# Optimization experiments

Hardware: AMD Instinct MI355X
Metric: run time of the kernel (lower is better)

## Reference

```python
import jax, jax.numpy as jnp
import numpy as np

N_NODES = 50000
N_EDGES = 400000
D = 64        # hidden_features
H_NE = 16     # hidden_ne_features
L = 4         # num_layers
EPS = 1e-5


def _ln(z, g, b):
    # layer norm over feature dim
    mu = jnp.mean(z, axis=-1, keepdims=True)
    var = jnp.var(z, axis=-1, keepdims=True)
    return (z - mu) * jax.lax.rsqrt(var + EPS) * g + b


def setup_inputs() -> dict:
    key = jax.random.key(0)
    ks = iter(jax.random.split(key, 64))
    def rn(shape, s=0.05):
        return jax.random.normal(next(ks), shape, dtype=jnp.float32) * s
    inp = {
        "x": rn((N_NODES, 2), 1.0),
        "e": rn((N_EDGES, 2), 1.0),
        "src": jax.random.randint(next(ks), (N_EDGES,), 0, N_NODES, dtype=jnp.int32),
        "dst": jax.random.randint(next(ks), (N_EDGES,), 0, N_NODES, dtype=jnp.int32),
        # node / edge encoders (2-layer MLPs)
        "ne_W1": rn((2, H_NE)), "ne_b1": jnp.zeros((H_NE,), jnp.float32),
        "ne_W2": rn((H_NE, D)), "ne_b2": jnp.zeros((D,), jnp.float32),
        "ee_W1": rn((2, H_NE)), "ee_b1": jnp.zeros((H_NE,), jnp.float32),
        "ee_W2": rn((H_NE, D)), "ee_b2": jnp.zeros((D,), jnp.float32),
        # stacked per-layer GatedGCN weights
        "A1": rn((L, D, D)), "bA1": jnp.zeros((L, D), jnp.float32),
        "A2": rn((L, D, D)), "bA2": jnp.zeros((L, D), jnp.float32),
        "A3": rn((L, D, D)), "bA3": jnp.zeros((L, D), jnp.float32),
        "B1": rn((L, D, D)), "bB1": jnp.zeros((L, D), jnp.float32),
        "B2": rn((L, D, D)), "bB2": jnp.zeros((L, D), jnp.float32),
        "B3": rn((L, D, D)), "bB3": jnp.zeros((L, D), jnp.float32),
        "ge": jnp.ones((L, D), jnp.float32), "be": jnp.zeros((L, D), jnp.float32),
        "gh": jnp.ones((L, D), jnp.float32), "bh": jnp.zeros((L, D), jnp.float32),
        # score predictor
        "pW1": rn((3 * D, D)), "pb1": jnp.zeros((D,), jnp.float32),
        "pW2": rn((D, 1)), "pb2": jnp.zeros((1,), jnp.float32),
    }
    return inp


def _forward(x, e, src, dst,
             ne_W1, ne_b1, ne_W2, ne_b2,
             ee_W1, ee_b1, ee_W2, ee_b2,
             A1, bA1, A2, bA2, A3, bA3,
             B1, bB1, B2, bB2, B3, bB3,
             ge, be, gh, bh,
             pW1, pb1, pW2, pb2):
    # encoders
    x = jax.nn.relu(x @ ne_W1 + ne_b1) @ ne_W2 + ne_b2      # [N, D]
    e = jax.nn.relu(e @ ee_W1 + ee_b1) @ ee_W2 + ee_b2      # [E, D]

    params = {"A1": A1, "bA1": bA1, "A2": A2, "bA2": bA2,
              "A3": A3, "bA3": bA3, "B1": B1, "bB1": bB1,
              "B2": B2, "bB2": bB2, "B3": B3, "bB3": bB3,
              "ge": ge, "be": be, "gh": gh, "bh": bh}

    def layer(carry, p):
        x, e = carry
        # edge update: e_ij += ReLU(LN(B1 h_i + B2 h_j + B3 e_ij))
        e_hat = (x[src] @ p["B1"] + p["bB1"]
                 + x[dst] @ p["B2"] + p["bB2"]
                 + e @ p["B3"] + p["bB3"])                  # [E, D]
        e = e + jax.nn.relu(_ln(e_hat, p["ge"], p["be"]))
        sigma = jax.nn.sigmoid(e)                             # gates [E, D]
        # directed aggregation: forward (src->dst) and backward (dst->src)
        a2 = x @ p["A2"] + p["bA2"]
        a3 = x @ p["A3"] + p["bA3"]
        m_f = jax.ops.segment_sum(sigma * a2[src], dst, num_segments=N_NODES)
        d_f = jax.ops.segment_sum(sigma, dst, num_segments=N_NODES)
        m_b = jax.ops.segment_sum(sigma * a3[dst], src, num_segments=N_NODES)
        d_b = jax.ops.segment_sum(sigma, src, num_segments=N_NODES)
        h = (x @ p["A1"] + p["bA1"]
             + m_f / (d_f + EPS) + m_b / (d_b + EPS))        # [N, D]
        x = x + jax.nn.relu(_ln(h, p["gh"], p["bh"]))
        return (x, e), None

    (x, e), _ = jax.lax.scan(layer, (x, e), params)

    # score predictor: MLP over cat(x_src, x_dst, e)
    z = jnp.concatenate([x[src], x[dst], e], axis=-1)        # [E, 3D]
    return jax.nn.relu(z @ pW1 + pb1) @ pW2 + pb2            # [E, 1]


def reference(x, e, src, dst,
              ne_W1, ne_b1, ne_W2, ne_b2,
              ee_W1, ee_b1, ee_W2, ee_b2,
              A1, bA1, A2, bA2, A3, bA3,
              B1, bB1, B2, bB2, B3, bB3,
              ge, be, gh, bh,
              pW1, pb1, pW2, pb2):
    return _forward(x, e, src, dst,
                    ne_W1, ne_b1, ne_W2, ne_b2,
                    ee_W1, ee_b1, ee_W2, ee_b2,
                    A1, bA1, A2, bA2, A3, bA3,
                    B1, bB1, B2, bB2, B3, bB3,
                    ge, be, gh, bh,
                    pW1, pb1, pW2, pb2)
```

## Files before the change

kernel.cpp:

```cpp
#include <hip/hip_runtime.h>

#define N_NODES 50000
#define N_EDGES 400000
#define EPSV 1e-5f
#define SCAN_BLK 49
#define SCAN_PAD (49 * 1024)

__global__ __launch_bounds__(256) void encode_kernel(
    const float* __restrict__ in2, const float* __restrict__ W1,
    const float* __restrict__ b1, const float* __restrict__ W2,
    const float* __restrict__ b2, float* __restrict__ out, int nrows)
{
  int t = blockIdx.x * 256 + threadIdx.x;
  int row = t >> 4;
  int d0 = t & 15;
  if (row >= nrows) return;
  float x0 = in2[row * 2 + 0], x1 = in2[row * 2 + 1];
  float h[16];
#pragma unroll
  for (int j = 0; j < 16; ++j)
    h[j] = fmaxf(fmaf(x0, W1[j], fmaf(x1, W1[16 + j], b1[j])), 0.f);
#pragma unroll
  for (int q = 0; q < 4; ++q) {
    int d = d0 + q * 16;
    float a = b2[d];
#pragma unroll
    for (int j = 0; j < 16; ++j) a = fmaf(h[j], W2[j * 64 + d], a);
    out[(size_t)row * 64 + d] = a;
  }
}

__global__ __launch_bounds__(256) void encode_perm_kernel(
    const float* __restrict__ in2, const float* __restrict__ W1,
    const float* __restrict__ b1, const float* __restrict__ W2,
    const float* __restrict__ b2, const int2* __restrict__ csr_f,
    float* __restrict__ out)
{
  int t = blockIdx.x * 256 + threadIdx.x;
  int row = t >> 4;
  int d0 = t & 15;
  if (row >= N_EDGES) return;
  int orig = csr_f[row].x;
  float x0 = in2[orig * 2 + 0], x1 = in2[orig * 2 + 1];
  float h[16];
#pragma unroll
  for (int j = 0; j < 16; ++j)
    h[j] = fmaxf(fmaf(x0, W1[j], fmaf(x1, W1[16 + j], b1[j])), 0.f);
#pragma unroll
  for (int q = 0; q < 4; ++q) {
    int d = d0 + q * 16;
    float a = b2[d];
#pragma unroll
    for (int j = 0; j < 16; ++j) a = fmaf(h[j], W2[j * 64 + d], a);
    out[(size_t)row * 64 + d] = a;
  }
}

__global__ __launch_bounds__(256) void hist_kernel(
    const int* __restrict__ src, const int* __restrict__ dst,
    int* __restrict__ cnt_f, int* __restrict__ cnt_b)
{
  int t = blockIdx.x * 256 + threadIdx.x;
  if (t >= N_EDGES) return;
  atomicAdd(&cnt_f[dst[t]], 1);
  atomicAdd(&cnt_b[src[t]], 1);
}

__global__ __launch_bounds__(1024) void scanA_kernel(
    const int* __restrict__ cnt_f, const int* __restrict__ cnt_b,
    int* __restrict__ part, int* __restrict__ bsum)
{
  int dir = blockIdx.x / SCAN_BLK;
  int blk = blockIdx.x % SCAN_BLK;
  const int* cnt = dir ? cnt_b : cnt_f;
  int t = threadIdx.x;
  int idx = blk * 1024 + t;
  int v = (idx < N_NODES) ? cnt[idx] : 0;
  __shared__ int sh[1024];
  sh[t] = v;
  __syncthreads();
  for (int o = 1; o < 1024; o <<= 1) {
    int u = (t >= o) ? sh[t - o] : 0;
    __syncthreads();
    sh[t] += u;
    __syncthreads();
  }
  part[dir * SCAN_PAD + idx] = sh[t] - v;
  if (t == 1023) bsum[dir * SCAN_BLK + blk] = sh[1023];
}

__global__ __launch_bounds__(64) void scanB_kernel(
    int* __restrict__ bsum, int* __restrict__ off_f, int* __restrict__ off_b)
{
  int t = threadIdx.x;
  if (t < 2) {
    int* b = bsum + t * SCAN_BLK;
    int run = 0;
    for (int i = 0; i < SCAN_BLK; ++i) {
      int v = b[i];
      b[i] = run;
      run += v;
    }
    if (t == 0) off_f[N_NODES] = run;
    else off_b[N_NODES] = run;
  }
}

__global__ __launch_bounds__(1024) void scanC_kernel(
    const int* __restrict__ part, const int* __restrict__ bsum,
    int* __restrict__ off_f, int* __restrict__ off_b,
    int* __restrict__ cur_f, int* __restrict__ cur_b)
{
  int dir = blockIdx.x / SCAN_BLK;
  int blk = blockIdx.x % SCAN_BLK;
  int t = threadIdx.x;
  int idx = blk * 1024 + t;
  if (idx >= N_NODES) return;
  int v = part[dir * SCAN_PAD + idx] + bsum[dir * SCAN_BLK + blk];
  if (dir == 0) { off_f[idx] = v; cur_f[idx] = v; }
  else { off_b[idx] = v; cur_b[idx] = v; }
}

__global__ __launch_bounds__(256) void fill_kernel(
    const int* __restrict__ src, const int* __restrict__ dst,
    int* __restrict__ cur_f, int* __restrict__ cur_b,
    int2* __restrict__ csr_f, int2* __restrict__ csr_b)
{
  int t = blockIdx.x * 256 + threadIdx.x;
  if (t >= N_EDGES) return;
  int dv = dst[t], sv = src[t];
  int p = atomicAdd(&cur_f[dv], 1);
  csr_f[p] = make_int2(t, sv);
  int q = atomicAdd(&cur_b[sv], 1);
  csr_b[q] = make_int2(t, dv);
}

__global__ __launch_bounds__(256) void sort_kernel(
    const int* __restrict__ off_f, const int* __restrict__ off_b,
    int2* __restrict__ csr_f, int2* __restrict__ csr_b)
{
  int t = blockIdx.x * 256 + threadIdx.x;
  int n;
  int2* csr;
  const int* off;
  if (t < N_NODES) { n = t; csr = csr_f; off = off_f; }
  else if (t < 2 * N_NODES) { n = t - N_NODES; csr = csr_b; off = off_b; }
  else return;
  int b = off[n], e = off[n + 1];
  for (int i = b + 1; i < e; ++i) {
    int2 key = csr[i];
    int j = i - 1;
    while (j >= b && csr[j].x > key.x) { csr[j + 1] = csr[j]; --j; }
    csr[j + 1] = key;
  }
}

__global__ __launch_bounds__(256) void aux_inv_kernel(
    const int2* __restrict__ csr_f, int* __restrict__ inv_f)
{
  int p = blockIdx.x * 256 + threadIdx.x;
  if (p >= N_EDGES) return;
  inv_f[csr_f[p].x] = p;
}

__global__ __launch_bounds__(256) void aux_dst_kernel(
    const int* __restrict__ off_f, int* __restrict__ dst_f)
{
  int n = blockIdx.x * 256 + threadIdx.x;
  if (n >= N_NODES) return;
  int b = off_f[n], e = off_f[n + 1];
  for (int p = b; p < e; ++p) dst_f[p] = n;
}

__global__ __launch_bounds__(256) void aux_remap_kernel(
    const int* __restrict__ inv_f, int2* __restrict__ csr_b)
{
  int q = blockIdx.x * 256 + threadIdx.x;
  if (q >= N_EDGES) return;
  int2 c = csr_b[q];
  csr_b[q] = make_int2(inv_f[c.x], c.y);
}


__global__ __launch_bounds__(256, 4) void node_gemm_kernel(
    const float* __restrict__ X,
    const float* __restrict__ A1, const float* __restrict__ A2,
    const float* __restrict__ A3, const float* __restrict__ B1,
    const float* __restrict__ B2,
    const float* __restrict__ bA1, const float* __restrict__ bA2,
    const float* __restrict__ bA3, const float* __restrict__ bB1,
    const float* __restrict__ bB2,
    float* __restrict__ NA, int l)
{
  __shared__ float ett[4][64 * 36];
  const int NT = 1563;
  int wid = threadIdx.x >> 6;
  int lane = threadIdx.x & 63;
  int wf = blockIdx.x * 4 + wid;
  if (wf >= 5 * NT) return;
  int m = wf / NT;
  int t = wf - m * NT;
  int row0 = t * 32;
  int r8 = lane & 7, c8 = lane >> 3;
  int col = 8 * c8;
  float* tl = ett[wid];
#pragma unroll
  for (int rb = 0; rb < 8; ++rb) {
    int r = row0 + 4 * rb;
    float v0 = (r + 0 < N_NODES) ? X[(size_t)(r + 0) * 64 + lane] : 0.f;
    float v1 = (r + 1 < N_NODES) ? X[(size_t)(r + 1) * 64 + lane] : 0.f;
    float v2 = (r + 2 < N_NODES) ? X[(size_t)(r + 2) * 64 + lane] : 0.f;
    float v3 = (r + 3 < N_NODES) ? X[(size_t)(r + 3) * 64 + lane] : 0.f;
    *reinterpret_cast<float4*>(&tl[lane * 36 + 4 * rb]) =
        make_float4(v0, v1, v2, v3);
  }
  const float* W;
  const float* bb;
  if (m == 0) { W = A1; bb = bA1; }
  else if (m == 1) { W = A2; bb = bA2; }
  else if (m == 2) { W = A3; bb = bA3; }
  else if (m == 3) { W = B1; bb = bB1; }
  else { W = B2; bb = bB2; }
  W += l * 64 * 64;
  float acc[4][8];
#pragma unroll
  for (int i = 0; i < 4; ++i)
#pragma unroll
    for (int j = 0; j < 8; ++j) acc[i][j] = 0.f;
#pragma unroll 8
  for (int k = 0; k < 64; ++k) {
    float4 er = *reinterpret_cast<const float4*>(&tl[k * 36 + 4 * r8]);
    float4 w0 = *reinterpret_cast<const float4*>(&W[k * 64 + col]);
    float4 w1 = *reinterpret_cast<const float4*>(&W[k * 64 + col + 4]);
    float ev[4] = {er.x, er.y, er.z, er.w};
    float wv[8] = {w0.x, w0.y, w0.z, w0.w, w1.x, w1.y, w1.z, w1.w};
#pragma unroll
    for (int i = 0; i < 4; ++i)
#pragma unroll
      for (int j = 0; j < 8; ++j) acc[i][j] = fmaf(ev[i], wv[j], acc[i][j]);
  }
  float4 b0 = *reinterpret_cast<const float4*>(&bb[l * 64 + col]);
  float4 b1 = *reinterpret_cast<const float4*>(&bb[l * 64 + col + 4]);
  float* out = NA + (size_t)m * N_NODES * 64;
#pragma unroll
  for (int i = 0; i < 4; ++i) {
    int row = row0 + 4 * r8 + i;
    if (row < N_NODES) {
      *reinterpret_cast<float4*>(&out[(size_t)row * 64 + col]) =
          make_float4(acc[i][0] + b0.x, acc[i][1] + b0.y, acc[i][2] + b0.z,
                      acc[i][3] + b0.w);
      *reinterpret_cast<float4*>(&out[(size_t)row * 64 + col + 4]) =
          make_float4(acc[i][4] + b1.x, acc[i][5] + b1.y, acc[i][6] + b1.z,
                      acc[i][7] + b1.w);
    }
  }
}

__global__ __launch_bounds__(256, 4) void edge_update_kernel(
    const float* __restrict__ NA,
    const float* __restrict__ B3, const float* __restrict__ bB3,
    const float* __restrict__ ge, const float* __restrict__ be,
    const int2* __restrict__ csr_f, const int* __restrict__ dst_f,
    float* __restrict__ E64, int l)
{
  __shared__ float ett[4][64 * 36];
  int wid = threadIdx.x >> 6;
  int lane = threadIdx.x & 63;
  int tile = blockIdx.x * 4 + wid;
  int e0 = tile * 32;
  int r8 = lane & 7, c8 = lane >> 3;
  int col = 8 * c8;
  float* tl = ett[wid];
#pragma unroll
  for (int rb = 0; rb < 8; ++rb) {
    int r = e0 + 4 * rb;
    float v0 = E64[(size_t)(r + 0) * 64 + lane];
    float v1 = E64[(size_t)(r + 1) * 64 + lane];
    float v2 = E64[(size_t)(r + 2) * 64 + lane];
    float v3 = E64[(size_t)(r + 3) * 64 + lane];
    *reinterpret_cast<float4*>(&tl[lane * 36 + 4 * rb]) =
        make_float4(v0, v1, v2, v3);
  }
  const float* W = B3 + l * 64 * 64;
  float acc[4][8];
#pragma unroll
  for (int i = 0; i < 4; ++i)
#pragma unroll
    for (int j = 0; j < 8; ++j) acc[i][j] = 0.f;
#pragma unroll 8
  for (int k = 0; k < 64; ++k) {
    float4 er = *reinterpret_cast<const float4*>(&tl[k * 36 + 4 * r8]);
    float4 w0 = *reinterpret_cast<const float4*>(&W[k * 64 + col]);
    float4 w1 = *reinterpret_cast<const float4*>(&W[k * 64 + col + 4]);
    float ev[4] = {er.x, er.y, er.z, er.w};
    float wv[8] = {w0.x, w0.y, w0.z, w0.w, w1.x, w1.y, w1.z, w1.w};
#pragma unroll
    for (int i = 0; i < 4; ++i)
#pragma unroll
      for (int j = 0; j < 8; ++j) acc[i][j] = fmaf(ev[i], wv[j], acc[i][j]);
  }
  const float* b1x = NA + (size_t)3 * N_NODES * 64;
  const float* b2x = NA + (size_t)4 * N_NODES * 64;
  float4 t0, t1;
  t0 = *reinterpret_cast<const float4*>(&bB3[l * 64 + col]);
  t1 = *reinterpret_cast<const float4*>(&bB3[l * 64 + col + 4]);
  float bbv[8] = {t0.x, t0.y, t0.z, t0.w, t1.x, t1.y, t1.z, t1.w};
  t0 = *reinterpret_cast<const float4*>(&ge[l * 64 + col]);
  t1 = *reinterpret_cast<const float4*>(&ge[l * 64 + col + 4]);
  float gev[8] = {t0.x, t0.y, t0.z, t0.w, t1.x, t1.y, t1.z, t1.w};
  t0 = *reinterpret_cast<const float4*>(&be[l * 64 + col]);
  t1 = *reinterpret_cast<const float4*>(&be[l * 64 + col + 4]);
  float bev[8] = {t0.x, t0.y, t0.z, t0.w, t1.x, t1.y, t1.z, t1.w};
#pragma unroll
  for (int i = 0; i < 4; ++i) {
    int row = e0 + 4 * r8 + i;
    int sv = csr_f[row].y;
    int dv = dst_f[row];
    float4 g0 = *reinterpret_cast<const float4*>(&b1x[(size_t)sv * 64 + col]);
    float4 g1 = *reinterpret_cast<const float4*>(&b1x[(size_t)sv * 64 + col + 4]);
    float4 h0 = *reinterpret_cast<const float4*>(&b2x[(size_t)dv * 64 + col]);
    float4 h1 = *reinterpret_cast<const float4*>(&b2x[(size_t)dv * 64 + col + 4]);
    float4 o0 = *reinterpret_cast<const float4*>(&E64[(size_t)row * 64 + col]);
    float4 o1 = *reinterpret_cast<const float4*>(&E64[(size_t)row * 64 + col + 4]);
    float g1v[8] = {g0.x, g0.y, g0.z, g0.w, g1.x, g1.y, g1.z, g1.w};
    float g2v[8] = {h0.x, h0.y, h0.z, h0.w, h1.x, h1.y, h1.z, h1.w};
    float eov[8] = {o0.x, o0.y, o0.z, o0.w, o1.x, o1.y, o1.z, o1.w};
    float z[8];
    float s1 = 0.f, s2 = 0.f;
#pragma unroll
    for (int j = 0; j < 8; ++j) {
      z[j] = acc[i][j] + bbv[j] + g1v[j] + g2v[j];
      s1 += z[j];
      s2 = fmaf(z[j], z[j], s2);
    }
    s1 += __shfl_xor(s1, 8, 64);  s2 += __shfl_xor(s2, 8, 64);
    s1 += __shfl_xor(s1, 16, 64); s2 += __shfl_xor(s2, 16, 64);
    s1 += __shfl_xor(s1, 32, 64); s2 += __shfl_xor(s2, 32, 64);
    float mean = s1 * (1.f / 64.f);
    float var = fmaxf(s2 * (1.f / 64.f) - mean * mean, 0.f);
    float rstd = rsqrtf(var + EPSV);
    float o[8];
#pragma unroll
    for (int j = 0; j < 8; ++j)
      o[j] = eov[j] + fmaxf(fmaf((z[j] - mean) * rstd, gev[j], bev[j]), 0.f);
    *reinterpret_cast<float4*>(&E64[(size_t)row * 64 + col]) =
        make_float4(o[0], o[1], o[2], o[3]);
    *reinterpret_cast<float4*>(&E64[(size_t)row * 64 + col + 4]) =
        make_float4(o[4], o[5], o[6], o[7]);
  }
}

__global__ __launch_bounds__(256) void aggregate_kernel(
    const float* __restrict__ NA, const float* __restrict__ E64,
    const int* __restrict__ off_f, const int* __restrict__ off_b,
    const int2* __restrict__ csr_f, const int2* __restrict__ csr_b,
    const float* __restrict__ gh, const float* __restrict__ bh,
    float* __restrict__ X, int l)
{
  int wave = threadIdx.x >> 6;
  int lane = threadIdx.x & 63;
  int n = blockIdx.x * 4 + wave;
  if (n >= N_NODES) return;
  const float* A1x = NA;
  const float* A2x = NA + (size_t)N_NODES * 64;
  const float* A3x = NA + (size_t)2 * N_NODES * 64;
  float xo = X[(size_t)n * 64 + lane];
  float a1v = A1x[(size_t)n * 64 + lane];
  float ghv = gh[l * 64 + lane];
  float bhv = bh[l * 64 + lane];
  int pf = off_f[n], pfe = off_f[n + 1];
  int pb = off_b[n], pbe = off_b[n + 1];
  float mf = 0.f, df = 0.f, mb = 0.f, db = 0.f;
  bool hf = pf < pfe, hb = pb < pbe;
  float evf = 0.f, avf = 0.f, evb = 0.f, avb = 0.f;
  if (hf) {
    evf = E64[(size_t)pf * 64 + lane];
    avf = A2x[(size_t)csr_f[pf].y * 64 + lane];
  }
  if (hb) {
    int2 c = csr_b[pb];
    evb = E64[(size_t)c.x * 64 + lane];
    avb = A3x[(size_t)c.y * 64 + lane];
  }
  while (hf || hb) {
    bool nf = (pf + 1) < pfe;
    bool nb = (pb + 1) < pbe;
    float evf2 = 0.f, avf2 = 0.f, evb2 = 0.f, avb2 = 0.f;
    if (nf) {
      evf2 = E64[(size_t)(pf + 1) * 64 + lane];
      avf2 = A2x[(size_t)csr_f[pf + 1].y * 64 + lane];
    }
    if (nb) {
      int2 c = csr_b[pb + 1];
      evb2 = E64[(size_t)c.x * 64 + lane];
      avb2 = A3x[(size_t)c.y * 64 + lane];
    }
    if (hf) {
      float sg = __builtin_amdgcn_rcpf(1.f + __expf(-evf));
      mf = fmaf(sg, avf, mf);
      df += sg;
      ++pf;
      evf = evf2;
      avf = avf2;
      hf = nf;
    }
    if (hb) {
      float sg = __builtin_amdgcn_rcpf(1.f + __expf(-evb));
      mb = fmaf(sg, avb, mb);
      db += sg;
      ++pb;
      evb = evb2;
      avb = avb2;
      hb = nb;
    }
  }
  float h = a1v + mf * __builtin_amdgcn_rcpf(df + EPSV) +
            mb * __builtin_amdgcn_rcpf(db + EPSV);
  float s1 = h, s2 = h * h;
#pragma unroll
  for (int m = 1; m < 64; m <<= 1) {
    s1 += __shfl_xor(s1, m, 64);
    s2 += __shfl_xor(s2, m, 64);
  }
  float mean = s1 * (1.f / 64.f);
  float var = fmaxf(s2 * (1.f / 64.f) - mean * mean, 0.f);
  float rstd = rsqrtf(var + EPSV);
  X[(size_t)n * 64 + lane] =
      xo + fmaxf(fmaf((h - mean) * rstd, ghv, bhv), 0.f);
}

__global__ __launch_bounds__(256, 4) void pred_node_kernel(
    const float* __restrict__ X, const float* __restrict__ pW1,
    float* __restrict__ U, float* __restrict__ V)
{
  __shared__ float ett[4][64 * 36];
  const int NT = 1563;
  int wid = threadIdx.x >> 6;
  int lane = threadIdx.x & 63;
  int wf = blockIdx.x * 4 + wid;
  if (wf >= 2 * NT) return;
  int m = wf / NT;
  int t = wf - m * NT;
  int row0 = t * 32;
  int r8 = lane & 7, c8 = lane >> 3;
  int col = 8 * c8;
  float* tl = ett[wid];
#pragma unroll
  for (int rb = 0; rb < 8; ++rb) {
    int r = row0 + 4 * rb;
    float v0 = (r + 0 < N_NODES) ? X[(size_t)(r + 0) * 64 + lane] : 0.f;
    float v1 = (r + 1 < N_NODES) ? X[(size_t)(r + 1) * 64 + lane] : 0.f;
    float v2 = (r + 2 < N_NODES) ? X[(size_t)(r + 2) * 64 + lane] : 0.f;
    float v3 = (r + 3 < N_NODES) ? X[(size_t)(r + 3) * 64 + lane] : 0.f;
    *reinterpret_cast<float4*>(&tl[lane * 36 + 4 * rb]) =
        make_float4(v0, v1, v2, v3);
  }
  const float* W = pW1 + (size_t)m * 64 * 64;
  float acc[4][8];
#pragma unroll
  for (int i = 0; i < 4; ++i)
#pragma unroll
    for (int j = 0; j < 8; ++j) acc[i][j] = 0.f;
#pragma unroll 8
  for (int k = 0; k < 64; ++k) {
    float4 er = *reinterpret_cast<const float4*>(&tl[k * 36 + 4 * r8]);
    float4 w0 = *reinterpret_cast<const float4*>(&W[k * 64 + col]);
    float4 w1 = *reinterpret_cast<const float4*>(&W[k * 64 + col + 4]);
    float ev[4] = {er.x, er.y, er.z, er.w};
    float wv[8] = {w0.x, w0.y, w0.z, w0.w, w1.x, w1.y, w1.z, w1.w};
#pragma unroll
    for (int i = 0; i < 4; ++i)
#pragma unroll
      for (int j = 0; j < 8; ++j) acc[i][j] = fmaf(ev[i], wv[j], acc[i][j]);
  }
  float* out = m ? V : U;
#pragma unroll
  for (int i = 0; i < 4; ++i) {
    int row = row0 + 4 * r8 + i;
    if (row < N_NODES) {
      *reinterpret_cast<float4*>(&out[(size_t)row * 64 + col]) =
          make_float4(acc[i][0], acc[i][1], acc[i][2], acc[i][3]);
      *reinterpret_cast<float4*>(&out[(size_t)row * 64 + col + 4]) =
          make_float4(acc[i][4], acc[i][5], acc[i][6], acc[i][7]);
    }
  }
}

__global__ __launch_bounds__(256, 4) void pred_edge_kernel(
    const float* __restrict__ U, const float* __restrict__ V,
    const float* __restrict__ E64,
    const int2* __restrict__ csr_f, const int* __restrict__ dst_f,
    const float* __restrict__ pW1, const float* __restrict__ pb1,
    const float* __restrict__ pW2, const float* __restrict__ pb2,
    float* __restrict__ out)
{
  __shared__ float ett[4][64 * 36];
  int wid = threadIdx.x >> 6;
  int lane = threadIdx.x & 63;
  int tile = blockIdx.x * 4 + wid;
  int e0 = tile * 32;
  int r8 = lane & 7, c8 = lane >> 3;
  int col = 8 * c8;
  float* tl = ett[wid];
#pragma unroll
  for (int rb = 0; rb < 8; ++rb) {
    int r = e0 + 4 * rb;
    float v0 = E64[(size_t)(r + 0) * 64 + lane];
    float v1 = E64[(size_t)(r + 1) * 64 + lane];
    float v2 = E64[(size_t)(r + 2) * 64 + lane];
    float v3 = E64[(size_t)(r + 3) * 64 + lane];
    *reinterpret_cast<float4*>(&tl[lane * 36 + 4 * rb]) =
        make_float4(v0, v1, v2, v3);
  }
  const float* W = pW1 + (size_t)128 * 64;
  float acc[4][8];
#pragma unroll
  for (int i = 0; i < 4; ++i)
#pragma unroll
    for (int j = 0; j < 8; ++j) acc[i][j] = 0.f;
#pragma unroll 8
  for (int k = 0; k < 64; ++k) {
    float4 er = *reinterpret_cast<const float4*>(&tl[k * 36 + 4 * r8]);
    float4 w0 = *reinterpret_cast<const float4*>(&W[k * 64 + col]);
    float4 w1 = *reinterpret_cast<const float4*>(&W[k * 64 + col + 4]);
    float ev[4] = {er.x, er.y, er.z, er.w};
    float wv[8] = {w0.x, w0.y, w0.z, w0.w, w1.x, w1.y, w1.z, w1.w};
#pragma unroll
    for (int i = 0; i < 4; ++i)
#pragma unroll
      for (int j = 0; j < 8; ++j) acc[i][j] = fmaf(ev[i], wv[j], acc[i][j]);
  }
  float4 t0, t1;
  t0 = *reinterpret_cast<const float4*>(&pb1[col]);
  t1 = *reinterpret_cast<const float4*>(&pb1[col + 4]);
  float pb1v[8] = {t0.x, t0.y, t0.z, t0.w, t1.x, t1.y, t1.z, t1.w};
  t0 = *reinterpret_cast<const float4*>(&pW2[col]);
  t1 = *reinterpret_cast<const float4*>(&pW2[col + 4]);
  float pw2v[8] = {t0.x, t0.y, t0.z, t0.w, t1.x, t1.y, t1.z, t1.w};
  float pb2v = pb2[0];
#pragma unroll
  for (int i = 0; i < 4; ++i) {
    int row = e0 + 4 * r8 + i;
    int2 cf = csr_f[row];
    int sv = cf.y;
    int dv = dst_f[row];
    float4 g0 = *reinterpret_cast<const float4*>(&U[(size_t)sv * 64 + col]);
    float4 g1 = *reinterpret_cast<const float4*>(&U[(size_t)sv * 64 + col + 4]);
    float4 h0 = *reinterpret_cast<const float4*>(&V[(size_t)dv * 64 + col]);
    float4 h1 = *reinterpret_cast<const float4*>(&V[(size_t)dv * 64 + col + 4]);
    float g1v[8] = {g0.x, g0.y, g0.z, g0.w, g1.x, g1.y, g1.z, g1.w};
    float g2v[8] = {h0.x, h0.y, h0.z, h0.w, h1.x, h1.y, h1.z, h1.w};
    float hsum = 0.f;
#pragma unroll
    for (int j = 0; j < 8; ++j) {
      float z = acc[i][j] + pb1v[j] + g1v[j] + g2v[j];
      hsum = fmaf(fmaxf(z, 0.f), pw2v[j], hsum);
    }
    hsum += __shfl_xor(hsum, 8, 64);
    hsum += __shfl_xor(hsum, 16, 64);
    hsum += __shfl_xor(hsum, 32, 64);
    if (c8 == 0) out[cf.x] = hsum + pb2v;
  }
}

extern "C" void kernel_launch(void* const* d_in, const int* in_sizes, int n_in,
                              void* d_out, int out_size, void* d_ws, size_t ws_size,
                              hipStream_t stream)
{
  const float* x = (const float*)d_in[0];
  const float* e = (const float*)d_in[1];
  const int* src = (const int*)d_in[2];
  const int* dst = (const int*)d_in[3];
  const float* neW1 = (const float*)d_in[4];
  const float* neb1 = (const float*)d_in[5];
  const float* neW2 = (const float*)d_in[6];
  const float* neb2 = (const float*)d_in[7];
  const float* eeW1 = (const float*)d_in[8];
  const float* eeb1 = (const float*)d_in[9];
  const float* eeW2 = (const float*)d_in[10];
  const float* eeb2 = (const float*)d_in[11];
  const float* A1 = (const float*)d_in[12];
  const float* bA1 = (const float*)d_in[13];
  const float* A2 = (const float*)d_in[14];
  const float* bA2 = (const float*)d_in[15];
  const float* A3 = (const float*)d_in[16];
  const float* bA3 = (const float*)d_in[17];
  const float* B1 = (const float*)d_in[18];
  const float* bB1 = (const float*)d_in[19];
  const float* B2 = (const float*)d_in[20];
  const float* bB2 = (const float*)d_in[21];
  const float* B3 = (const float*)d_in[22];
  const float* bB3 = (const float*)d_in[23];
  const float* ge = (const float*)d_in[24];
  const float* be = (const float*)d_in[25];
  const float* gh = (const float*)d_in[26];
  const float* bh = (const float*)d_in[27];
  const float* pW1 = (const float*)d_in[28];
  const float* pb1 = (const float*)d_in[29];
  const float* pW2 = (const float*)d_in[30];
  const float* pb2 = (const float*)d_in[31];

  char* ws = (char*)d_ws;
  float* X = (float*)ws;      ws += (size_t)N_NODES * 64 * 4;
  float* NA = (float*)ws;     ws += (size_t)5 * N_NODES * 64 * 4;
  float* E64 = (float*)ws;    ws += (size_t)N_EDGES * 64 * 4;
  int* cnt_f = (int*)ws;      ws += (size_t)N_NODES * 4;
  int* cnt_b = (int*)ws;      ws += (size_t)N_NODES * 4;
  int* off_f = (int*)ws;      ws += (size_t)(N_NODES + 1) * 4;
  int* off_b = (int*)ws;      ws += (size_t)(N_NODES + 1) * 4;
  int* cur_f = (int*)ws;      ws += (size_t)N_NODES * 4;
  int* cur_b = (int*)ws;      ws += (size_t)N_NODES * 4;
  int2* csr_f = (int2*)ws;    ws += (size_t)N_EDGES * 8;
  int2* csr_b = (int2*)ws;    ws += (size_t)N_EDGES * 8;
  int* part = (int*)ws;       ws += (size_t)2 * SCAN_PAD * 4;
  int* bsum = (int*)ws;       ws += (size_t)2 * SCAN_BLK * 4;
  int* inv_f = (int*)ws;      ws += (size_t)N_EDGES * 4;
  int* dst_f = (int*)ws;      ws += (size_t)N_EDGES * 4;
  float* U = NA + (size_t)3 * N_NODES * 64;
  float* V = NA + (size_t)4 * N_NODES * 64;

  hipMemsetAsync(cnt_f, 0, (size_t)2 * N_NODES * 4, stream);
  hist_kernel<<<(N_EDGES + 255) / 256, 256, 0, stream>>>(src, dst, cnt_f, cnt_b);
  scanA_kernel<<<2 * SCAN_BLK, 1024, 0, stream>>>(cnt_f, cnt_b, part, bsum);
  scanB_kernel<<<1, 64, 0, stream>>>(bsum, off_f, off_b);
  scanC_kernel<<<2 * SCAN_BLK, 1024, 0, stream>>>(part, bsum, off_f, off_b,
                                                  cur_f, cur_b);
  fill_kernel<<<(N_EDGES + 255) / 256, 256, 0, stream>>>(src, dst, cur_f, cur_b,
                                                         csr_f, csr_b);
  sort_kernel<<<(2 * N_NODES + 255) / 256, 256, 0, stream>>>(off_f, off_b, csr_f,
                                                             csr_b);
  aux_inv_kernel<<<(N_EDGES + 255) / 256, 256, 0, stream>>>(csr_f, inv_f);
  aux_dst_kernel<<<(N_NODES + 255) / 256, 256, 0, stream>>>(off_f, dst_f);
  aux_remap_kernel<<<(N_EDGES + 255) / 256, 256, 0, stream>>>(inv_f, csr_b);

  encode_kernel<<<(N_NODES * 16 + 255) / 256, 256, 0, stream>>>(
      x, neW1, neb1, neW2, neb2, X, N_NODES);
  encode_perm_kernel<<<(N_EDGES * 16 + 255) / 256, 256, 0, stream>>>(
      e, eeW1, eeb1, eeW2, eeb2, csr_f, E64);

  const int NGB = (5 * 1563 + 3) / 4;
  const int PNB = (2 * 1563 + 3) / 4;
  for (int l = 0; l < 4; ++l) {
    node_gemm_kernel<<<NGB, 256, 0, stream>>>(
        X, A1, A2, A3, B1, B2, bA1, bA2, bA3, bB1, bB2, NA, l);
    edge_update_kernel<<<N_EDGES / 128, 256, 0, stream>>>(NA, B3, bB3, ge, be,
                                                          csr_f, dst_f, E64, l);
    aggregate_kernel<<<(N_NODES + 3) / 4, 256, 0, stream>>>(
        NA, E64, off_f, off_b, csr_f, csr_b, gh, bh, X, l);
  }

  pred_node_kernel<<<PNB, 256, 0, stream>>>(X, pW1, U, V);
  pred_edge_kernel<<<N_EDGES / 128, 256, 0, stream>>>(U, V, E64, csr_f, dst_f,
                                                      pW1, pb1, pW2, pb2,
                                                      (float*)d_out);
}
```

Baseline: 1.277 ms.

## Share node tile across weight matrices, split src index array, simplify aggregate loops

The node GEMM and predictor-node kernels now load one 32-row X tile per block into shared memory with coalesced float4 reads. Each wavefront applies a different weight matrix to that shared tile, so X is read once instead of five (or two) times. A compact src_f int array replaces the int2 csr_f reads in the edge update and forward aggregation, halving index traffic. The aggregate kernel's hand-pipelined interleaved loop becomes two simple unrolled loops, and the bsum scan uses wave shuffles instead of a serial loop. The risks are that the aggregate loses its explicit prefetch overlap and that the 320-thread blocks change occupancy.

```diff
diff --git a/kernel.cpp b/kernel.cpp
--- a/kernel.cpp
+++ b/kernel.cpp
@@ -89,20 +89,22 @@
   if (t == 1023) bsum[dir * SCAN_BLK + blk] = sh[1023];
 }
 
-__global__ __launch_bounds__(64) void scanB_kernel(
+__global__ __launch_bounds__(128) void scanB_kernel(
     int* __restrict__ bsum, int* __restrict__ off_f, int* __restrict__ off_b)
 {
-  int t = threadIdx.x;
-  if (t < 2) {
-    int* b = bsum + t * SCAN_BLK;
-    int run = 0;
-    for (int i = 0; i < SCAN_BLK; ++i) {
-      int v = b[i];
-      b[i] = run;
-      run += v;
-    }
-    if (t == 0) off_f[N_NODES] = run;
-    else off_b[N_NODES] = run;
+  int dir = threadIdx.x >> 6;
+  int i = threadIdx.x & 63;
+  int v = (i < SCAN_BLK) ? bsum[dir * SCAN_BLK + i] : 0;
+  int s = v;
+#pragma unroll
+  for (int o = 1; o < 64; o <<= 1) {
+    int u = __shfl_up(s, o, 64);
+    if (i >= o) s += u;
+  }
+  if (i < SCAN_BLK) bsum[dir * SCAN_BLK + i] = s - v;
+  if (i == SCAN_BLK - 1) {
+    if (dir == 0) off_f[N_NODES] = s;
+    else off_b[N_NODES] = s;
   }
 }
 
@@ -156,11 +158,14 @@
 }
 
 __global__ __launch_bounds__(256) void aux_inv_kernel(
-    const int2* __restrict__ csr_f, int* __restrict__ inv_f)
+    const int2* __restrict__ csr_f, int* __restrict__ inv_f,
+    int* __restrict__ src_f)
 {
   int p = blockIdx.x * 256 + threadIdx.x;
   if (p >= N_EDGES) return;
-  inv_f[csr_f[p].x] = p;
+  int2 c = csr_f[p];
+  inv_f[c.x] = p;
+  src_f[p] = c.y;
 }
 
 __global__ __launch_bounds__(256) void aux_dst_kernel(
@@ -182,7 +187,7 @@
 }
 
 
-__global__ __launch_bounds__(256, 4) void node_gemm_kernel(
+__global__ __launch_bounds__(320, 6) void node_gemm_kernel(
     const float* __restrict__ X,
     const float* __restrict__ A1, const float* __restrict__ A2,
     const float* __restrict__ A3, const float* __restrict__ B1,
@@ -192,34 +197,30 @@
     const float* __restrict__ bB2,
     float* __restrict__ NA, int l)
 {
-  __shared__ float ett[4][64 * 36];
-  const int NT = 1563;
+  __shared__ float tl[64 * 36];
   int wid = threadIdx.x >> 6;
   int lane = threadIdx.x & 63;
-  int wf = blockIdx.x * 4 + wid;
-  if (wf >= 5 * NT) return;
-  int m = wf / NT;
-  int t = wf - m * NT;
-  int row0 = t * 32;
+  int row0 = blockIdx.x * 32;
+  for (int i = threadIdx.x; i < 32 * 16; i += 320) {
+    int r = i >> 4, c4 = (i & 15) * 4;
+    int row = row0 + r;
+    float4 v = (row < N_NODES)
+                   ? *reinterpret_cast<const float4*>(&X[(size_t)row * 64 + c4])
+                   : make_float4(0.f, 0.f, 0.f, 0.f);
+    tl[(c4 + 0) * 36 + r] = v.x;
+    tl[(c4 + 1) * 36 + r] = v.y;
+    tl[(c4 + 2) * 36 + r] = v.z;
+    tl[(c4 + 3) * 36 + r] = v.w;
+  }
+  __syncthreads();
   int r8 = lane & 7, c8 = lane >> 3;
   int col = 8 * c8;
-  float* tl = ett[wid];
-#pragma unroll
-  for (int rb = 0; rb < 8; ++rb) {
-    int r = row0 + 4 * rb;
-    float v0 = (r + 0 < N_NODES) ? X[(size_t)(r + 0) * 64 + lane] : 0.f;
-    float v1 = (r + 1 < N_NODES) ? X[(size_t)(r + 1) * 64 + lane] : 0.f;
-    float v2 = (r + 2 < N_NODES) ? X[(size_t)(r + 2) * 64 + lane] : 0.f;
-    float v3 = (r + 3 < N_NODES) ? X[(size_t)(r + 3) * 64 + lane] : 0.f;
-    *reinterpret_cast<float4*>(&tl[lane * 36 + 4 * rb]) =
-        make_float4(v0, v1, v2, v3);
-  }
   const float* W;
   const float* bb;
-  if (m == 0) { W = A1; bb = bA1; }
-  else if (m == 1) { W = A2; bb = bA2; }
-  else if (m == 2) { W = A3; bb = bA3; }
-  else if (m == 3) { W = B1; bb = bB1; }
+  if (wid == 0) { W = A1; bb = bA1; }
+  else if (wid == 1) { W = A2; bb = bA2; }
+  else if (wid == 2) { W = A3; bb = bA3; }
+  else if (wid == 3) { W = B1; bb = bB1; }
   else { W = B2; bb = bB2; }
   W += l * 64 * 64;
   float acc[4][8];
@@ -241,7 +242,7 @@
   }
   float4 b0 = *reinterpret_cast<const float4*>(&bb[l * 64 + col]);
   float4 b1 = *reinterpret_cast<const float4*>(&bb[l * 64 + col + 4]);
-  float* out = NA + (size_t)m * N_NODES * 64;
+  float* out = NA + (size_t)wid * N_NODES * 64;
 #pragma unroll
   for (int i = 0; i < 4; ++i) {
     int row = row0 + 4 * r8 + i;
@@ -260,7 +261,7 @@
     const float* __restrict__ NA,
     const float* __restrict__ B3, const float* __restrict__ bB3,
     const float* __restrict__ ge, const float* __restrict__ be,
-    const int2* __restrict__ csr_f, const int* __restrict__ dst_f,
+    const int* __restrict__ src_f, const int* __restrict__ dst_f,
     float* __restrict__ E64, int l)
 {
   __shared__ float ett[4][64 * 36];
@@ -314,7 +315,7 @@
 #pragma unroll
   for (int i = 0; i < 4; ++i) {
     int row = e0 + 4 * r8 + i;
-    int sv = csr_f[row].y;
+    int sv = src_f[row];
     int dv = dst_f[row];
     float4 g0 = *reinterpret_cast<const float4*>(&b1x[(size_t)sv * 64 + col]);
     float4 g1 = *reinterpret_cast<const float4*>(&b1x[(size_t)sv * 64 + col + 4]);
@@ -353,7 +354,7 @@
 __global__ __launch_bounds__(256) void aggregate_kernel(
     const float* __restrict__ NA, const float* __restrict__ E64,
     const int* __restrict__ off_f, const int* __restrict__ off_b,
-    const int2* __restrict__ csr_f, const int2* __restrict__ csr_b,
+    const int* __restrict__ src_f, const int2* __restrict__ csr_b,
     const float* __restrict__ gh, const float* __restrict__ bh,
     float* __restrict__ X, int l)
 {
@@ -371,48 +372,22 @@
   int pf = off_f[n], pfe = off_f[n + 1];
   int pb = off_b[n], pbe = off_b[n + 1];
   float mf = 0.f, df = 0.f, mb = 0.f, db = 0.f;
-  bool hf = pf < pfe, hb = pb < pbe;
-  float evf = 0.f, avf = 0.f, evb = 0.f, avb = 0.f;
-  if (hf) {
-    evf = E64[(size_t)pf * 64 + lane];
-    avf = A2x[(size_t)csr_f[pf].y * 64 + lane];
-  }
-  if (hb) {
-    int2 c = csr_b[pb];
-    evb = E64[(size_t)c.x * 64 + lane];
-    avb = A3x[(size_t)c.y * 64 + lane];
-  }
-  while (hf || hb) {
-    bool nf = (pf + 1) < pfe;
-    bool nb = (pb + 1) < pbe;
-    float evf2 = 0.f, avf2 = 0.f, evb2 = 0.f, avb2 = 0.f;
-    if (nf) {
-      evf2 = E64[(size_t)(pf + 1) * 64 + lane];
-      avf2 = A2x[(size_t)csr_f[pf + 1].y * 64 + lane];
-    }
-    if (nb) {
-      int2 c = csr_b[pb + 1];
-      evb2 = E64[(size_t)c.x * 64 + lane];
-      avb2 = A3x[(size_t)c.y * 64 + lane];
-    }
-    if (hf) {
-      float sg = __builtin_amdgcn_rcpf(1.f + __expf(-evf));
-      mf = fmaf(sg, avf, mf);
-      df += sg;
-      ++pf;
-      evf = evf2;
-      avf = avf2;
-      hf = nf;
-    }
-    if (hb) {
-      float sg = __builtin_amdgcn_rcpf(1.f + __expf(-evb));
-      mb = fmaf(sg, avb, mb);
-      db += sg;
-      ++pb;
-      evb = evb2;
-      avb = avb2;
-      hb = nb;
-    }
+#pragma unroll 4
+  for (int p = pf; p < pfe; ++p) {
+    float ev = E64[(size_t)p * 64 + lane];
+    float av = A2x[(size_t)src_f[p] * 64 + lane];
+    float sg = __builtin_amdgcn_rcpf(1.f + __expf(-ev));
+    mf = fmaf(sg, av, mf);
+    df += sg;
+  }
+#pragma unroll 4
+  for (int p = pb; p < pbe; ++p) {
+    int2 c = csr_b[p];
+    float ev = E64[(size_t)c.x * 64 + lane];
+    float av = A3x[(size_t)c.y * 64 + lane];
+    float sg = __builtin_amdgcn_rcpf(1.f + __expf(-ev));
+    mb = fmaf(sg, av, mb);
+    db += sg;
   }
   float h = a1v + mf * __builtin_amdgcn_rcpf(df + EPSV) +
             mb * __builtin_amdgcn_rcpf(db + EPSV);
@@ -429,33 +404,29 @@
       xo + fmaxf(fmaf((h - mean) * rstd, ghv, bhv), 0.f);
 }
 
-__global__ __launch_bounds__(256, 4) void pred_node_kernel(
+__global__ __launch_bounds__(128, 8) void pred_node_kernel(
     const float* __restrict__ X, const float* __restrict__ pW1,
     float* __restrict__ U, float* __restrict__ V)
 {
-  __shared__ float ett[4][64 * 36];
-  const int NT = 1563;
+  __shared__ float tl[64 * 36];
   int wid = threadIdx.x >> 6;
   int lane = threadIdx.x & 63;
-  int wf = blockIdx.x * 4 + wid;
-  if (wf >= 2 * NT) return;
-  int m = wf / NT;
-  int t = wf - m * NT;
-  int row0 = t * 32;
+  int row0 = blockIdx.x * 32;
+  for (int i = threadIdx.x; i < 32 * 16; i += 128) {
+    int r = i >> 4, c4 = (i & 15) * 4;
+    int row = row0 + r;
+    float4 v = (row < N_NODES)
+                   ? *reinterpret_cast<const float4*>(&X[(size_t)row * 64 + c4])
+                   : make_float4(0.f, 0.f, 0.f, 0.f);
+    tl[(c4 + 0) * 36 + r] = v.x;
+    tl[(c4 + 1) * 36 + r] = v.y;
+    tl[(c4 + 2) * 36 + r] = v.z;
+    tl[(c4 + 3) * 36 + r] = v.w;
+  }
+  __syncthreads();
   int r8 = lane & 7, c8 = lane >> 3;
   int col = 8 * c8;
-  float* tl = ett[wid];
-#pragma unroll
-  for (int rb = 0; rb < 8; ++rb) {
-    int r = row0 + 4 * rb;
-    float v0 = (r + 0 < N_NODES) ? X[(size_t)(r + 0) * 64 + lane] : 0.f;
-    float v1 = (r + 1 < N_NODES) ? X[(size_t)(r + 1) * 64 + lane] : 0.f;
-    float v2 = (r + 2 < N_NODES) ? X[(size_t)(r + 2) * 64 + lane] : 0.f;
-    float v3 = (r + 3 < N_NODES) ? X[(size_t)(r + 3) * 64 + lane] : 0.f;
-    *reinterpret_cast<float4*>(&tl[lane * 36 + 4 * rb]) =
-        make_float4(v0, v1, v2, v3);
-  }
-  const float* W = pW1 + (size_t)m * 64 * 64;
+  const float* W = pW1 + (size_t)wid * 64 * 64;
   float acc[4][8];
 #pragma unroll
   for (int i = 0; i < 4; ++i)
@@ -473,7 +444,7 @@
 #pragma unroll
       for (int j = 0; j < 8; ++j) acc[i][j] = fmaf(ev[i], wv[j], acc[i][j]);
   }
-  float* out = m ? V : U;
+  float* out = wid ? V : U;
 #pragma unroll
   for (int i = 0; i < 4; ++i) {
     int row = row0 + 4 * r8 + i;
@@ -616,20 +587,21 @@
   int* bsum = (int*)ws;       ws += (size_t)2 * SCAN_BLK * 4;
   int* inv_f = (int*)ws;      ws += (size_t)N_EDGES * 4;
   int* dst_f = (int*)ws;      ws += (size_t)N_EDGES * 4;
+  int* src_f = (int*)ws;      ws += (size_t)N_EDGES * 4;
   float* U = NA + (size_t)3 * N_NODES * 64;
   float* V = NA + (size_t)4 * N_NODES * 64;
 
   hipMemsetAsync(cnt_f, 0, (size_t)2 * N_NODES * 4, stream);
   hist_kernel<<<(N_EDGES + 255) / 256, 256, 0, stream>>>(src, dst, cnt_f, cnt_b);
   scanA_kernel<<<2 * SCAN_BLK, 1024, 0, stream>>>(cnt_f, cnt_b, part, bsum);
-  scanB_kernel<<<1, 64, 0, stream>>>(bsum, off_f, off_b);
+  scanB_kernel<<<1, 128, 0, stream>>>(bsum, off_f, off_b);
   scanC_kernel<<<2 * SCAN_BLK, 1024, 0, stream>>>(part, bsum, off_f, off_b,
                                                   cur_f, cur_b);
   fill_kernel<<<(N_EDGES + 255) / 256, 256, 0, stream>>>(src, dst, cur_f, cur_b,
                                                          csr_f, csr_b);
   sort_kernel<<<(2 * N_NODES + 255) / 256, 256, 0, stream>>>(off_f, off_b, csr_f,
                                                              csr_b);
-  aux_inv_kernel<<<(N_EDGES + 255) / 256, 256, 0, stream>>>(csr_f, inv_f);
+  aux_inv_kernel<<<(N_EDGES + 255) / 256, 256, 0, stream>>>(csr_f, inv_f, src_f);
   aux_dst_kernel<<<(N_NODES + 255) / 256, 256, 0, stream>>>(off_f, dst_f);
   aux_remap_kernel<<<(N_EDGES + 255) / 256, 256, 0, stream>>>(inv_f, csr_b);
 
@@ -638,18 +610,17 @@
   encode_perm_kernel<<<(N_EDGES * 16 + 255) / 256, 256, 0, stream>>>(
       e, eeW1, eeb1, eeW2, eeb2, csr_f, E64);
 
-  const int NGB = (5 * 1563 + 3) / 4;
-  const int PNB = (2 * 1563 + 3) / 4;
+  const int NT = (N_NODES + 31) / 32;
   for (int l = 0; l < 4; ++l) {
-    node_gemm_kernel<<<NGB, 256, 0, stream>>>(
+    node_gemm_kernel<<<NT, 320, 0, stream>>>(
         X, A1, A2, A3, B1, B2, bA1, bA2, bA3, bB1, bB2, NA, l);
     edge_update_kernel<<<N_EDGES / 128, 256, 0, stream>>>(NA, B3, bB3, ge, be,
-                                                          csr_f, dst_f, E64, l);
+                                                          src_f, dst_f, E64, l);
     aggregate_kernel<<<(N_NODES + 3) / 4, 256, 0, stream>>>(
-        NA, E64, off_f, off_b, csr_f, csr_b, gh, bh, X, l);
-  }
-
-  pred_node_kernel<<<PNB, 256, 0, stream>>>(X, pW1, U, V);
+        NA, E64, off_f, off_b, src_f, csr_b, gh, bh, X, l);
+  }
+
+  pred_node_kernel<<<NT, 128, 0, stream>>>(X, pW1, U, V);
   pred_edge_kernel<<<N_EDGES / 128, 256, 0, stream>>>(U, V, E64, csr_f, dst_f,
                                                       pW1, pb1, pW2, pb2,
                                                       (float*)d_out);
```

New measurement: 1.158 ms. 9.3% less time.
